# Performance work log

Measured on AMD Instinct MI355X. Metric: run time of the kernel, lower is better.

The kernel has to match this reference:

```python
import jax, jax.numpy as jnp
import numpy as np
from jax import lax

B, T = 4, 1024
V, C, H, L = 50257, 768, 12, 12
D = C // H           # head size = 64
FF = 4 * C           # ffn hidden = 3072
EPS = 1e-5


def setup_inputs() -> dict:
    key = jax.random.key(0)
    ks = jax.random.split(key, 20)
    s = 0.02
    inp = {
        'x': jax.random.randint(ks[0], (B, T), 0, V, dtype=jnp.int32),
        'y': jax.random.randint(ks[1], (B, T), 0, V, dtype=jnp.int32),
        'tok_emb': jax.random.normal(ks[2], (V, C), jnp.float32) * s,
        'pos_emb': jax.random.normal(ks[3], (V, C), jnp.float32) * s,
        'Wk': jax.random.normal(ks[4], (L, H, C, D), jnp.float32) * s,
        'Wq': jax.random.normal(ks[5], (L, H, C, D), jnp.float32) * s,
        'Wv': jax.random.normal(ks[6], (L, H, C, D), jnp.float32) * s,
        'Wproj': jax.random.normal(ks[7], (L, C, C), jnp.float32) * s,
        'bproj': jnp.zeros((L, C), jnp.float32),
        'ln1_g': jnp.ones((L, C), jnp.float32),
        'ln1_b': jnp.zeros((L, C), jnp.float32),
        'W1': jax.random.normal(ks[8], (L, C, FF), jnp.float32) * s,
        'b1': jnp.zeros((L, FF), jnp.float32),
        'W2': jax.random.normal(ks[9], (L, FF, C), jnp.float32) * s,
        'b2': jnp.zeros((L, C), jnp.float32),
        'ln2_g': jnp.ones((L, C), jnp.float32),
        'ln2_b': jnp.zeros((L, C), jnp.float32),
        'Wlm': jax.random.normal(ks[10], (C, V), jnp.float32) * s,
        'blm': jnp.zeros((V,), jnp.float32),
    }
    return inp


def _layernorm(x, g, b):
    m = jnp.mean(x, axis=-1, keepdims=True)
    v = jnp.var(x, axis=-1, keepdims=True)
    return (x - m) * lax.rsqrt(v + EPS) * g + b


def _forward(x, tok_emb, pos_emb, Wk, Wq, Wv, Wproj, bproj, ln1_g, ln1_b,
             W1, b1, W2, b2, ln2_g, ln2_b, Wlm, blm):
    # NOTE: the original indexes the position embedding table with token ids x.
    h = tok_emb[x] + pos_emb[x]                      # [B,T,C]
    mask = jnp.tril(jnp.ones((T, T), bool))          # causal tril buffer
    scale = D ** -0.5

    def layer(h, p):
        wk, wq, wv, wp, bp, g1, be1, w1, bb1, w2, bb2, g2, be2 = p
        k = jnp.einsum('btc,hcd->bhtd', h, wk)
        q = jnp.einsum('btc,hcd->bhtd', h, wq)
        v = jnp.einsum('btc,hcd->bhtd', h, wv)
        # faithful quirk: k @ q^T (rows=k index, cols=q index)
        wei = jnp.einsum('bhtd,bhsd->bhts', k, q) * scale
        wei = jnp.where(mask, wei, -jnp.inf)
        wei = jax.nn.softmax(wei, axis=-1)
        o = jnp.einsum('bhts,bhsd->bhtd', wei, v)    # [B,H,T,D]
        o = o.transpose(0, 2, 1, 3).reshape(B, T, C) # concat heads
        attn = o @ wp + bp
        h = _layernorm(h + attn, g1, be1)
        ff = jax.nn.relu(h @ w1 + bb1) @ w2 + bb2
        h = _layernorm(h + ff, g2, be2)
        return h, None

    params = (Wk, Wq, Wv, Wproj, bproj, ln1_g, ln1_b, W1, b1, W2, b2, ln2_g, ln2_b)
    h, _ = lax.scan(layer, h, params)
    logits = h @ Wlm + blm                           # [B,T,V]
    return logits


def reference(x, y, tok_emb, pos_emb, Wk, Wq, Wv, Wproj, bproj, ln1_g, ln1_b,
              W1, b1, W2, b2, ln2_g, ln2_b, Wlm, blm):
    logits = _forward(x, tok_emb, pos_emb, Wk, Wq, Wv, Wproj, bproj,
                      ln1_g, ln1_b, W1, b1, W2, b2, ln2_g, ln2_b, Wlm, blm)
    logp = jax.nn.log_softmax(logits, axis=-1)
    loss = -jnp.mean(jnp.take_along_axis(logp, y[..., None].astype(jnp.int32), axis=-1))
    return logits, loss
```

## Files before the change

### kernel.cpp

```cpp
#include <hip/hip_runtime.h>
#include <hip/hip_bf16.h>
#include <math.h>

#define BB 4
#define TT 1024
#define VV 50257
#define VPAD2 50432
#define CC 768
#define HH 12
#define DD 64
#define LL 12
#define FFH 3072
#define MROWS (BB*TT)
#define QBLK 128
#define KVBLK 64
#define NPART (VPAD2 / 64)

typedef __bf16 bf16x8 __attribute__((ext_vector_type(8)));
typedef float  f32x4  __attribute__((ext_vector_type(4)));
typedef unsigned int u32;
#define AS1 __attribute__((address_space(1)))
#define AS3 __attribute__((address_space(3)))

static __device__ __forceinline__ void gload_lds16(const void* g, void* l) {
    __builtin_amdgcn_global_load_lds((const AS1 u32*)g, (AS3 u32*)l, 16, 0, 0);
}

static __device__ __forceinline__ void stage_tile(const __hip_bfloat16* __restrict__ A,
                                                  const __hip_bfloat16* __restrict__ Bt,
                                                  int Kld, int k0, int bm, int bn,
                                                  int w, int l, char* As, char* Bs) {
    #pragma unroll
    for (int it = 0; it < 4; it++) {
        int chunk = w * 4 + it;
        int o = chunk * 1024 + l * 16;
        int row = o >> 7;
        int cb = (o & 127) ^ ((row & 7) << 4);
        gload_lds16(A + (size_t)(bm + row) * Kld + k0 + (cb >> 1), As + chunk * 1024);
        gload_lds16(Bt + (size_t)(bn + row) * Kld + k0 + (cb >> 1), Bs + chunk * 1024);
    }
}

static __device__ __forceinline__ void stage_tile256(const __hip_bfloat16* __restrict__ A,
                                                     const __hip_bfloat16* __restrict__ Bt,
                                                     int Kld, int k0, int bm, int bn,
                                                     int w, int l, char* As, char* Bs) {
    #pragma unroll
    for (int it = 0; it < 4; it++) {
        int chunk = w * 4 + it;
        int o = chunk * 1024 + l * 16;
        int row = o >> 7;
        int cb = (o & 127) ^ ((row & 7) << 4);
        gload_lds16(A + (size_t)(bm + row) * Kld + k0 + (cb >> 1), As + chunk * 1024);
        gload_lds16(Bt + (size_t)(bn + row) * Kld + k0 + (cb >> 1), Bs + chunk * 1024);
    }
}

__global__ void embed_kernel(const int* __restrict__ x, const float* __restrict__ tok,
                             const float* __restrict__ pos, float* __restrict__ h,
                             __hip_bfloat16* __restrict__ hb) {
    int idx = blockIdx.x * 256 + threadIdx.x;
    if (idx >= MROWS * CC) return;
    int row = idx / CC, c = idx - row * CC;
    int id = x[row];
    float v = tok[(size_t)id * CC + c] + pos[(size_t)id * CC + c];
    h[idx] = v;
    hb[idx] = __float2bfloat16(v);
}

__global__ __launch_bounds__(256) void cvtT_mat(const float* __restrict__ in,
                                                __hip_bfloat16* __restrict__ out,
                                                int K, int Nin,
                                                size_t ibs, size_t obs) {
    __shared__ float t[32][33];
    const float* ip = in + blockIdx.z * ibs;
    __hip_bfloat16* op = out + blockIdx.z * obs;
    int n0 = blockIdx.x * 32, k0 = blockIdx.y * 32;
    int tx = threadIdx.x & 31, ty = threadIdx.x >> 5;
    #pragma unroll
    for (int i = 0; i < 4; i++) {
        int k = k0 + ty + i * 8, n = n0 + tx;
        t[ty + i * 8][tx] = (n < Nin) ? ip[(size_t)k * Nin + n] : 0.f;
    }
    __syncthreads();
    #pragma unroll
    for (int i = 0; i < 4; i++) {
        int n = n0 + ty + i * 8, k = k0 + tx;
        op[(size_t)n * K + k] = __float2bfloat16(t[tx][ty + i * 8]);
    }
}

__global__ __launch_bounds__(256) void cvtT_qkv(const float* __restrict__ Wk,
                                                const float* __restrict__ Wq,
                                                const float* __restrict__ Wv,
                                                __hip_bfloat16* __restrict__ kT,
                                                __hip_bfloat16* __restrict__ qT,
                                                __hip_bfloat16* __restrict__ vT) {
    int z = blockIdx.z;
    int tensor = z / 144, lh = z % 144;
    int l = lh / HH, hh = lh % HH;
    const float* in = (tensor == 0 ? Wk : tensor == 1 ? Wq : Wv) + (size_t)lh * CC * DD;
    __hip_bfloat16* out = (tensor == 0 ? kT : tensor == 1 ? qT : vT)
                          + ((size_t)l * CC + hh * DD) * CC;
    __shared__ float t[32][33];
    int c0 = blockIdx.x * 32, d0 = blockIdx.y * 32;
    int tx = threadIdx.x & 31, ty = threadIdx.x >> 5;
    #pragma unroll
    for (int i = 0; i < 4; i++)
        t[ty + i * 8][tx] = in[(size_t)(c0 + ty + i * 8) * DD + d0 + tx];
    __syncthreads();
    #pragma unroll
    for (int i = 0; i < 4; i++)
        out[(size_t)(d0 + ty + i * 8) * CC + c0 + tx] = __float2bfloat16(t[tx][ty + i * 8]);
}

__global__ __launch_bounds__(256) void gemm_mfma(const __hip_bfloat16* __restrict__ A,
                                                 const __hip_bfloat16* __restrict__ Bt,
                                                 const float* __restrict__ bias,
                                                 float* __restrict__ Cf,
                                                 __hip_bfloat16* __restrict__ Cb,
                                                 int M, int N, int K, int relu) {
    __shared__ __align__(16) char smem[65536];
    int tid = threadIdx.x;
    int l = tid & 63, w = tid >> 6;
    int wr = w >> 1, wc = w & 1;
    int bm = blockIdx.y * 128, bn = blockIdx.x * 128;

    f32x4 acc[4][4] = {};

    stage_tile(A, Bt, K, 0, bm, bn, w, l, smem, smem + 32768);
    int p = 0;
    for (int k0 = 0; k0 < K; k0 += 64) {
        __syncthreads();
        if (k0 + 64 < K)
            stage_tile(A, Bt, K, k0 + 64, bm, bn, w, l,
                       smem + (p ^ 1) * 16384, smem + 32768 + (p ^ 1) * 16384);
        const char* Ab = smem + p * 16384;
        const char* Bb = smem + 32768 + p * 16384;
        #pragma unroll
        for (int ks = 0; ks < 2; ks++) {
            bf16x8 af[4], bfr[4];
            #pragma unroll
            for (int i = 0; i < 4; i++) {
                int row = wr * 64 + i * 16 + (l & 15);
                int cb = (ks * 64 + (l >> 4) * 16) ^ ((row & 7) << 4);
                af[i] = *(const bf16x8*)(Ab + row * 128 + cb);
            }
            #pragma unroll
            for (int j = 0; j < 4; j++) {
                int row = wc * 64 + j * 16 + (l & 15);
                int cb = (ks * 64 + (l >> 4) * 16) ^ ((row & 7) << 4);
                bfr[j] = *(const bf16x8*)(Bb + row * 128 + cb);
            }
            #pragma unroll
            for (int i = 0; i < 4; i++)
                #pragma unroll
                for (int j = 0; j < 4; j++)
                    acc[i][j] = __builtin_amdgcn_mfma_f32_16x16x32_bf16(af[i], bfr[j], acc[i][j], 0, 0, 0);
        }
        p ^= 1;
    }

    if (Cb) {
        __hip_bfloat16* ebh = (__hip_bfloat16*)smem;
        __syncthreads();
        #pragma unroll
        for (int i = 0; i < 4; i++) {
            #pragma unroll
            for (int j = 0; j < 4; j++) {
                int colt = wc * 64 + j * 16 + (l & 15);
                float bv = bias ? bias[bn + colt] : 0.f;
                #pragma unroll
                for (int r = 0; r < 4; r++) {
                    int rowc = wr * 64 + i * 16 + (l >> 4) * 4 + r;
                    float v = acc[i][j][r] + bv;
                    if (relu) v = fmaxf(v, 0.f);
                    ebh[rowc * 136 + colt] = __float2bfloat16(v);
                }
            }
        }
        __syncthreads();
        #pragma unroll
        for (int pass = 0; pass < 8; pass++) {
            int idx = pass * 256 + tid;
            int rowc = idx >> 4, colq = idx & 15;
            *(bf16x8*)&Cb[(size_t)(bm + rowc) * N + bn + colq * 8] =
                *(const bf16x8*)&ebh[rowc * 136 + colq * 8];
        }
    } else {
        float* eb = (float*)smem;
        #pragma unroll
        for (int c = 0; c < 2; c++) {
            __syncthreads();
            if (wr == c) {
                #pragma unroll
                for (int i = 0; i < 4; i++) {
                    #pragma unroll
                    for (int j = 0; j < 4; j++) {
                        int colt = wc * 64 + j * 16 + (l & 15);
                        float bv = bias ? bias[bn + colt] : 0.f;
                        #pragma unroll
                        for (int r = 0; r < 4; r++) {
                            int rowc = i * 16 + (l >> 4) * 4 + r;
                            float v = acc[i][j][r] + bv;
                            if (relu) v = fmaxf(v, 0.f);
                            eb[rowc * 132 + colt] = v;
                        }
                    }
                }
            }
            __syncthreads();
            #pragma unroll
            for (int pass = 0; pass < 8; pass++) {
                int idx = pass * 256 + tid;
                int rowc = idx >> 5, colq = idx & 31;
                *(f32x4*)&Cf[(size_t)(bm + c * 64 + rowc) * N + bn + colq * 4] =
                    *(const f32x4*)&eb[rowc * 132 + colq * 4];
            }
        }
    }
}

__global__ __launch_bounds__(512) void lm_head_mfma256(const __hip_bfloat16* __restrict__ A,
                                                       const __hip_bfloat16* __restrict__ Bt,
                                                       const float* __restrict__ bias,
                                                       float* __restrict__ Cf,
                                                       float* __restrict__ pm,
                                                       float* __restrict__ ps) {
    __shared__ __align__(16) char smem[131072];
    int tid = threadIdx.x;
    int l = tid & 63, w = tid >> 6;
    int wr = w >> 2, wc = w & 3;
    int bm = blockIdx.x * 256, bn = blockIdx.y * 256;

    f32x4 acc[8][4] = {};

    stage_tile256(A, Bt, CC, 0, bm, bn, w, l, smem, smem + 65536);
    int p = 0;
    for (int k0 = 0; k0 < CC; k0 += 64) {
        __syncthreads();
        if (k0 + 64 < CC)
            stage_tile256(A, Bt, CC, k0 + 64, bm, bn, w, l,
                          smem + (p ^ 1) * 32768, smem + 65536 + (p ^ 1) * 32768);
        const char* Ab = smem + p * 32768;
        const char* Bb = smem + 65536 + p * 32768;
        #pragma unroll
        for (int ks = 0; ks < 2; ks++) {
            bf16x8 af[8], bfr[4];
            #pragma unroll
            for (int i = 0; i < 8; i++) {
                int row = wr * 128 + i * 16 + (l & 15);
                int cb = (ks * 64 + (l >> 4) * 16) ^ ((row & 7) << 4);
                af[i] = *(const bf16x8*)(Ab + row * 128 + cb);
            }
            #pragma unroll
            for (int j = 0; j < 4; j++) {
                int row = wc * 64 + j * 16 + (l & 15);
                int cb = (ks * 64 + (l >> 4) * 16) ^ ((row & 7) << 4);
                bfr[j] = *(const bf16x8*)(Bb + row * 128 + cb);
            }
            #pragma unroll
            for (int i = 0; i < 8; i++)
                #pragma unroll
                for (int j = 0; j < 4; j++)
                    acc[i][j] = __builtin_amdgcn_mfma_f32_16x16x32_bf16(af[i], bfr[j], acc[i][j], 0, 0, 0);
        }
        p ^= 1;
    }

    #pragma unroll
    for (int j = 0; j < 4; j++) {
        int col = bn + wc * 64 + j * 16 + (l & 15);
        float bv = (col < VV) ? bias[col] : 0.f;
        #pragma unroll
        for (int i = 0; i < 8; i++)
            #pragma unroll
            for (int r = 0; r < 4; r++)
                acc[i][j][r] += bv;
    }

    int pidx = blockIdx.y * 4 + wc;
    #pragma unroll
    for (int i = 0; i < 8; i++) {
        int row = bm + wr * 128 + i * 16 + (l >> 4) * 4;
        #pragma unroll
        for (int r = 0; r < 4; r++) {
            float pv[4];
            float rmax = -1e30f;
            #pragma unroll
            for (int j = 0; j < 4; j++) {
                int col = bn + wc * 64 + j * 16 + (l & 15);
                float v = (col < VV) ? acc[i][j][r] : -1e30f;
                pv[j] = v;
                rmax = fmaxf(rmax, v);
            }
            #pragma unroll
            for (int msk = 1; msk < 16; msk <<= 1)
                rmax = fmaxf(rmax, __shfl_xor(rmax, msk));
            float s = 0.f;
            #pragma unroll
            for (int j = 0; j < 4; j++) s += __expf(pv[j] - rmax);
            #pragma unroll
            for (int msk = 1; msk < 16; msk <<= 1)
                s += __shfl_xor(s, msk);
            if ((l & 15) == 0) {
                pm[(size_t)(row + r) * NPART + pidx] = rmax;
                ps[(size_t)(row + r) * NPART + pidx] = s;
            }
        }
    }

    float* eb = (float*)smem;
    #pragma unroll
    for (int c = 0; c < 4; c++) {
        __syncthreads();
        if (wr == (c >> 1)) {
            int i0 = (c & 1) * 4;
            #pragma unroll
            for (int i = 0; i < 4; i++) {
                #pragma unroll
                for (int j = 0; j < 4; j++) {
                    int colt = wc * 64 + j * 16 + (l & 15);
                    #pragma unroll
                    for (int r = 0; r < 4; r++) {
                        int rowc = i * 16 + (l >> 4) * 4 + r;
                        eb[rowc * 264 + colt] = acc[i0 + i][j][r];
                    }
                }
            }
        }
        __syncthreads();
        #pragma unroll
        for (int pass = 0; pass < 32; pass++) {
            int idx = pass * 512 + tid;
            int rowc = idx >> 8, colq = idx & 255;
            int col = bn + colq;
            if (col < VV)
                Cf[(size_t)(bm + c * 64 + rowc) * VV + col] = eb[rowc * 264 + colq];
        }
    }
}

__global__ __launch_bounds__(256) void nll_combine(const float* __restrict__ pm,
                                                   const float* __restrict__ ps,
                                                   const float* __restrict__ logits,
                                                   const int* __restrict__ y,
                                                   float* __restrict__ rl) {
    int m = blockIdx.x, tid = threadIdx.x;
    __shared__ float rm[256], rs[256];
    float mt = -1e30f, st = 0.f;
    for (int i = tid; i < NPART; i += 256) {
        float mi = pm[(size_t)m * NPART + i];
        float si = ps[(size_t)m * NPART + i];
        float mn = fmaxf(mt, mi);
        st = st * __expf(mt - mn) + si * __expf(mi - mn);
        mt = mn;
    }
    rm[tid] = mt; rs[tid] = st; __syncthreads();
    for (int off = 128; off > 0; off >>= 1) {
        if (tid < off) {
            float ma = rm[tid], mb = rm[tid + off];
            float mn = fmaxf(ma, mb);
            rs[tid] = rs[tid] * __expf(ma - mn) + rs[tid + off] * __expf(mb - mn);
            rm[tid] = mn;
        }
        __syncthreads();
    }
    if (tid == 0)
        rl[m] = logf(rs[0]) + rm[0] - logits[(size_t)m * VV + y[m]];
}

__global__ __launch_bounds__(256) void gemm_qkv_mfma(const __hip_bfloat16* __restrict__ A,
                                                     const __hip_bfloat16* __restrict__ kT,
                                                     const __hip_bfloat16* __restrict__ qT,
                                                     const __hip_bfloat16* __restrict__ vT,
                                                     __hip_bfloat16* __restrict__ ko,
                                                     __hip_bfloat16* __restrict__ qo,
                                                     __hip_bfloat16* __restrict__ vto) {
    const __hip_bfloat16* Bt = (blockIdx.z == 0) ? kT : (blockIdx.z == 1) ? qT : vT;
    __shared__ __align__(16) char smem[65536];
    int tid = threadIdx.x;
    int l = tid & 63, w = tid >> 6;
    int wr = w >> 1, wc = w & 1;
    int bm = blockIdx.y * 128, bn = blockIdx.x * 128;

    f32x4 acc[4][4] = {};

    stage_tile(A, Bt, CC, 0, bm, bn, w, l, smem, smem + 32768);
    int p = 0;
    for (int k0 = 0; k0 < CC; k0 += 64) {
        __syncthreads();
        if (k0 + 64 < CC)
            stage_tile(A, Bt, CC, k0 + 64, bm, bn, w, l,
                       smem + (p ^ 1) * 16384, smem + 32768 + (p ^ 1) * 16384);
        const char* Ab = smem + p * 16384;
        const char* Bb = smem + 32768 + p * 16384;
        #pragma unroll
        for (int ks = 0; ks < 2; ks++) {
            bf16x8 af[4], bfr[4];
            #pragma unroll
            for (int i = 0; i < 4; i++) {
                int row = wr * 64 + i * 16 + (l & 15);
                int cb = (ks * 64 + (l >> 4) * 16) ^ ((row & 7) << 4);
                af[i] = *(const bf16x8*)(Ab + row * 128 + cb);
            }
            #pragma unroll
            for (int j = 0; j < 4; j++) {
                int row = wc * 64 + j * 16 + (l & 15);
                int cb = (ks * 64 + (l >> 4) * 16) ^ ((row & 7) << 4);
                bfr[j] = *(const bf16x8*)(Bb + row * 128 + cb);
            }
            #pragma unroll
            for (int i = 0; i < 4; i++)
                #pragma unroll
                for (int j = 0; j < 4; j++)
                    acc[i][j] = __builtin_amdgcn_mfma_f32_16x16x32_bf16(af[i], bfr[j], acc[i][j], 0, 0, 0);
        }
        p ^= 1;
    }
    int zz = blockIdx.z;
    #pragma unroll
    for (int i = 0; i < 4; i++) {
        int row = bm + wr * 64 + i * 16 + (l >> 4) * 4;
        #pragma unroll
        for (int j = 0; j < 4; j++) {
            int col = bn + wc * 64 + j * 16 + (l & 15);
            int head = col >> 6, d = col & 63;
            #pragma unroll
            for (int r = 0; r < 4; r++) {
                int m = row + r;
                int b = m >> 10, t = m & 1023;
                __hip_bfloat16 val = __float2bfloat16(acc[i][j][r]);
                if (zz == 0)      ko[(((size_t)(b * HH + head)) * TT + t) * DD + d] = val;
                else if (zz == 1) qo[(((size_t)(b * HH + head)) * TT + t) * DD + d] = val;
                else              vto[(((size_t)(b * HH + head)) * DD + d) * TT + t] = val;
            }
        }
    }
}

__global__ __launch_bounds__(256) void attn_mfma(const __hip_bfloat16* __restrict__ kq,
                                                 const __hip_bfloat16* __restrict__ qk,
                                                 const __hip_bfloat16* __restrict__ vt,
                                                 __hip_bfloat16* __restrict__ oc) {
    __shared__ __hip_bfloat16 Qs[2][KVBLK * 64];
    __shared__ __hip_bfloat16 Vs[2][64 * KVBLK];
    __shared__ __hip_bfloat16 Ps[QBLK * KVBLK];
    int tid = threadIdx.x;
    int l = tid & 63, w = tid >> 6;
    int t0 = blockIdx.x * QBLK;
    size_t bh = (size_t)(blockIdx.z * HH + blockIdx.y);
    const __hip_bfloat16* kqp = kq + bh * TT * DD;
    const __hip_bfloat16* qkp = qk + bh * TT * DD;
    const __hip_bfloat16* vtp = vt + bh * DD * TT;

    bf16x8 af[2][2];
    #pragma unroll
    for (int i = 0; i < 2; i++)
        #pragma unroll
        for (int ks = 0; ks < 2; ks++)
            af[i][ks] = *(const bf16x8*)&kqp[(size_t)(t0 + w * 32 + i * 16 + (l & 15)) * DD
                                             + ks * 32 + (l >> 4) * 8];

    f32x4 acc_o[2][4] = {};
    float mrow[2][4], lrow[2][4];
    #pragma unroll
    for (int i = 0; i < 2; i++)
        #pragma unroll
        for (int r = 0; r < 4; r++) { mrow[i][r] = -1e30f; lrow[i][r] = 0.f; }

    auto stageKV = [&](int pp, int s0) {
        #pragma unroll
        for (int it = 0; it < 2; it++) {
            int chunk = w * 2 + it;
            int o = chunk * 1024 + l * 16;
            int row = o >> 7;
            int cb = (o & 127) ^ ((row & 7) << 4);
            gload_lds16(qkp + (size_t)(s0 + row) * DD + (cb >> 1),
                        (char*)Qs[pp] + chunk * 1024);
            gload_lds16(vtp + (size_t)row * TT + s0 + (cb >> 1),
                        (char*)Vs[pp] + chunk * 1024);
        }
    };

    int nt = (t0 + QBLK) / KVBLK;
    stageKV(0, 0);
    int p = 0;
    for (int ti = 0; ti < nt; ti++) {
        int s0 = ti * KVBLK;
        __syncthreads();
        if (ti + 1 < nt) stageKV(p ^ 1, s0 + KVBLK);

        f32x4 sa[2][4] = {};
        #pragma unroll
        for (int ks = 0; ks < 2; ks++) {
            bf16x8 bfr[4];
            #pragma unroll
            for (int j = 0; j < 4; j++) {
                int row = j * 16 + (l & 15);
                int cb = (ks * 64 + (l >> 4) * 16) ^ ((row & 7) << 4);
                bfr[j] = *(const bf16x8*)((const char*)Qs[p] + row * 128 + cb);
            }
            #pragma unroll
            for (int i = 0; i < 2; i++)
                #pragma unroll
                for (int j = 0; j < 4; j++)
                    sa[i][j] = __builtin_amdgcn_mfma_f32_16x16x32_bf16(af[i][ks], bfr[j], sa[i][j], 0, 0, 0);
        }

        #pragma unroll
        for (int i = 0; i < 2; i++) {
            #pragma unroll
            for (int r = 0; r < 4; r++) {
                int t = t0 + w * 32 + i * 16 + (l >> 4) * 4 + r;
                float pv[4];
                float rmax = -1e30f;
                #pragma unroll
                for (int j = 0; j < 4; j++) {
                    int s = s0 + j * 16 + (l & 15);
                    float v = sa[i][j][r] * 0.125f;
                    v = (s <= t) ? v : -1e30f;
                    pv[j] = v;
                    rmax = fmaxf(rmax, v);
                }
                #pragma unroll
                for (int msk = 1; msk < 16; msk <<= 1)
                    rmax = fmaxf(rmax, __shfl_xor(rmax, msk));
                float mo = mrow[i][r];
                float mn = fmaxf(mo, rmax);
                float fac = __expf(mo - mn);
                float ls = 0.f;
                int prow = w * 32 + i * 16 + (l >> 4) * 4 + r;
                #pragma unroll
                for (int j = 0; j < 4; j++) {
                    float e = __expf(pv[j] - mn);
                    ls += e;
                    int cb = (j * 32 + (l & 15) * 2) ^ ((prow & 7) << 4);
                    *(__hip_bfloat16*)((char*)Ps + prow * 128 + cb) = __float2bfloat16(e);
                }
                #pragma unroll
                for (int msk = 1; msk < 16; msk <<= 1)
                    ls += __shfl_xor(ls, msk);
                mrow[i][r] = mn;
                lrow[i][r] = lrow[i][r] * fac + ls;
                #pragma unroll
                for (int jd = 0; jd < 4; jd++)
                    acc_o[i][jd][r] *= fac;
            }
        }

        #pragma unroll
        for (int ks = 0; ks < 2; ks++) {
            bf16x8 pa[2], vf[4];
            #pragma unroll
            for (int i = 0; i < 2; i++) {
                int row = w * 32 + i * 16 + (l & 15);
                int cb = (ks * 64 + (l >> 4) * 16) ^ ((row & 7) << 4);
                pa[i] = *(const bf16x8*)((const char*)Ps + row * 128 + cb);
            }
            #pragma unroll
            for (int jd = 0; jd < 4; jd++) {
                int row = jd * 16 + (l & 15);
                int cb = (ks * 64 + (l >> 4) * 16) ^ ((row & 7) << 4);
                vf[jd] = *(const bf16x8*)((const char*)Vs[p] + row * 128 + cb);
            }
            #pragma unroll
            for (int i = 0; i < 2; i++)
                #pragma unroll
                for (int jd = 0; jd < 4; jd++)
                    acc_o[i][jd] = __builtin_amdgcn_mfma_f32_16x16x32_bf16(pa[i], vf[jd], acc_o[i][jd], 0, 0, 0);
        }
        p ^= 1;
    }

    int b = blockIdx.z, hh = blockIdx.y;
    #pragma unroll
    for (int i = 0; i < 2; i++) {
        #pragma unroll
        for (int r = 0; r < 4; r++) {
            float inv = 1.f / lrow[i][r];
            int t = t0 + w * 32 + i * 16 + (l >> 4) * 4 + r;
            #pragma unroll
            for (int jd = 0; jd < 4; jd++) {
                int d = jd * 16 + (l & 15);
                oc[((size_t)(b * TT + t)) * CC + hh * DD + d] =
                    __float2bfloat16(acc_o[i][jd][r] * inv);
            }
        }
    }
}

__global__ __launch_bounds__(256) void resid_ln(float* __restrict__ h,
                                                const float* __restrict__ t,
                                                const float* __restrict__ g,
                                                const float* __restrict__ bta,
                                                __hip_bfloat16* __restrict__ hb) {
    int row = blockIdx.x;
    int tid = threadIdx.x;
    __shared__ float red[256];
    float x[3];
    float s = 0.f;
    #pragma unroll
    for (int i = 0; i < 3; i++) {
        int c = tid + i * 256;
        x[i] = h[(size_t)row * CC + c] + t[(size_t)row * CC + c];
        s += x[i];
    }
    red[tid] = s; __syncthreads();
    for (int off = 128; off > 0; off >>= 1) {
        if (tid < off) red[tid] += red[tid + off];
        __syncthreads();
    }
    float mean = red[0] * (1.f / CC); __syncthreads();
    float s2 = 0.f;
    #pragma unroll
    for (int i = 0; i < 3; i++) { float dd = x[i] - mean; s2 += dd * dd; }
    red[tid] = s2; __syncthreads();
    for (int off = 128; off > 0; off >>= 1) {
        if (tid < off) red[tid] += red[tid + off];
        __syncthreads();
    }
    float inv = rsqrtf(red[0] * (1.f / CC) + 1e-5f);
    #pragma unroll
    for (int i = 0; i < 3; i++) {
        int c = tid + i * 256;
        float o = (x[i] - mean) * inv * g[c] + bta[c];
        h[(size_t)row * CC + c] = o;
        hb[(size_t)row * CC + c] = __float2bfloat16(o);
    }
}

__global__ __launch_bounds__(256) void loss_reduce(const float* __restrict__ rl,
                                                   float* __restrict__ out) {
    int tid = threadIdx.x;
    __shared__ float red[256];
    float s = 0.f;
    for (int i = tid; i < MROWS; i += 256) s += rl[i];
    red[tid] = s; __syncthreads();
    for (int off = 128; off > 0; off >>= 1) {
        if (tid < off) red[tid] += red[tid + off];
        __syncthreads();
    }
    if (tid == 0) out[0] = red[0] * (1.f / MROWS);
}

extern "C" void kernel_launch(void* const* d_in, const int* in_sizes, int n_in,
                              void* d_out, int out_size, void* d_ws, size_t ws_size,
                              hipStream_t stream) {
    const int*   x     = (const int*)d_in[0];
    const int*   y     = (const int*)d_in[1];
    const float* tok   = (const float*)d_in[2];
    const float* pos   = (const float*)d_in[3];
    const float* Wk    = (const float*)d_in[4];
    const float* Wq    = (const float*)d_in[5];
    const float* Wv    = (const float*)d_in[6];
    const float* Wproj = (const float*)d_in[7];
    const float* bproj = (const float*)d_in[8];
    const float* ln1g  = (const float*)d_in[9];
    const float* ln1b  = (const float*)d_in[10];
    const float* W1    = (const float*)d_in[11];
    const float* b1    = (const float*)d_in[12];
    const float* W2    = (const float*)d_in[13];
    const float* b2    = (const float*)d_in[14];
    const float* ln2g  = (const float*)d_in[15];
    const float* ln2b  = (const float*)d_in[16];
    const float* Wlm   = (const float*)d_in[17];
    const float* blm   = (const float*)d_in[18];

    float* logits = (float*)d_out;
    float* lossp  = (float*)d_out + ((size_t)out_size - 1);

    char* p = (char*)d_ws;
    auto alloc = [&](size_t bytes) { char* r = p; p += (bytes + 255) & ~255ULL; return r; };
    const size_t S_HC = (size_t)MROWS * CC;

    float* h    = (float*)alloc(S_HC * 4);
    float* tmpf = (float*)alloc(S_HC * 4);
    float* rl   = (float*)alloc(MROWS * 4);
    float* pm   = (float*)alloc((size_t)MROWS * NPART * 4);
    float* ps   = (float*)alloc((size_t)MROWS * NPART * 4);
    __hip_bfloat16* kbb  = (__hip_bfloat16*)alloc(S_HC * 2);
    __hip_bfloat16* qbb  = (__hip_bfloat16*)alloc(S_HC * 2);
    __hip_bfloat16* vtb  = (__hip_bfloat16*)alloc(S_HC * 2);
    __hip_bfloat16* hb   = (__hip_bfloat16*)alloc(S_HC * 2);
    __hip_bfloat16* ocb  = (__hip_bfloat16*)alloc(S_HC * 2);
    __hip_bfloat16* ff1b = (__hip_bfloat16*)alloc((size_t)MROWS * FFH * 2);
    __hip_bfloat16* kT   = (__hip_bfloat16*)alloc((size_t)LL * CC * CC * 2);
    __hip_bfloat16* qT   = (__hip_bfloat16*)alloc((size_t)LL * CC * CC * 2);
    __hip_bfloat16* vT   = (__hip_bfloat16*)alloc((size_t)LL * CC * CC * 2);
    __hip_bfloat16* pT   = (__hip_bfloat16*)alloc((size_t)LL * CC * CC * 2);
    __hip_bfloat16* w1T  = (__hip_bfloat16*)alloc((size_t)LL * CC * FFH * 2);
    __hip_bfloat16* w2T  = (__hip_bfloat16*)alloc((size_t)LL * FFH * CC * 2);
    __hip_bfloat16* lmT  = (__hip_bfloat16*)alloc((size_t)VPAD2 * CC * 2);

    dim3 blk(256);

    cvtT_qkv<<<dim3(24, 2, 3 * 144), blk, 0, stream>>>(Wk, Wq, Wv, kT, qT, vT);
    cvtT_mat<<<dim3(24, 24, LL), blk, 0, stream>>>(Wproj, pT, CC, CC,
                                                   (size_t)CC * CC, (size_t)CC * CC);
    cvtT_mat<<<dim3(96, 24, LL), blk, 0, stream>>>(W1, w1T, CC, FFH,
                                                   (size_t)CC * FFH, (size_t)FFH * CC);
    cvtT_mat<<<dim3(24, 96, LL), blk, 0, stream>>>(W2, w2T, FFH, CC,
                                                   (size_t)FFH * CC, (size_t)CC * FFH);
    cvtT_mat<<<dim3(VPAD2 / 32, 24, 1), blk, 0, stream>>>(Wlm, lmT, CC, VV, 0, 0);

    embed_kernel<<<dim3((MROWS * CC + 255) / 256), blk, 0, stream>>>(x, tok, pos, h, hb);

    for (int l = 0; l < LL; l++) {
        const __hip_bfloat16* kT_l = kT + (size_t)l * CC * CC;
        const __hip_bfloat16* qT_l = qT + (size_t)l * CC * CC;
        const __hip_bfloat16* vT_l = vT + (size_t)l * CC * CC;
        const __hip_bfloat16* pT_l = pT + (size_t)l * CC * CC;
        const __hip_bfloat16* w1T_l = w1T + (size_t)l * CC * FFH;
        const __hip_bfloat16* w2T_l = w2T + (size_t)l * FFH * CC;

        gemm_qkv_mfma<<<dim3(CC / 128, MROWS / 128, 3), blk, 0, stream>>>(
            hb, kT_l, qT_l, vT_l, kbb, qbb, vtb);
        attn_mfma<<<dim3(TT / QBLK, HH, BB), blk, 0, stream>>>(kbb, qbb, vtb, ocb);
        gemm_mfma<<<dim3(CC / 128, MROWS / 128), blk, 0, stream>>>(
            ocb, pT_l, bproj + (size_t)l * CC, tmpf, (__hip_bfloat16*)nullptr,
            MROWS, CC, CC, 0);
        resid_ln<<<dim3(MROWS), blk, 0, stream>>>(h, tmpf, ln1g + (size_t)l * CC,
                                                  ln1b + (size_t)l * CC, hb);
        gemm_mfma<<<dim3(FFH / 128, MROWS / 128), blk, 0, stream>>>(
            hb, w1T_l, b1 + (size_t)l * FFH, (float*)nullptr, ff1b,
            MROWS, FFH, CC, 1);
        gemm_mfma<<<dim3(CC / 128, MROWS / 128), blk, 0, stream>>>(
            ff1b, w2T_l, b2 + (size_t)l * CC, tmpf, (__hip_bfloat16*)nullptr,
            MROWS, CC, FFH, 0);
        resid_ln<<<dim3(MROWS), blk, 0, stream>>>(h, tmpf, ln2g + (size_t)l * CC,
                                                  ln2b + (size_t)l * CC, hb);
    }

    lm_head_mfma256<<<dim3(MROWS / 256, VPAD2 / 256), dim3(512), 0, stream>>>(
        hb, lmT, blm, logits, pm, ps);
    nll_combine<<<dim3(MROWS), blk, 0, stream>>>(pm, ps, logits, y, rl);
    loss_reduce<<<dim3(1), blk, 0, stream>>>(rl, lossp);
}
```

Before: 3.394 ms.

## Halve LM-head LDS with K=32 stages and stage QKV epilogue through LDS

The LM-head GEMM now stages 32-wide K slices instead of 64, cutting its shared memory from 128KB to 64KB. The smaller footprint may let two 512-thread blocks share a CU, at the cost of twice as many barriers per K loop and a narrower swizzle. Its output epilogue is rechunked to 32-row pieces so it fits in the smaller buffer. Separately, the QKV projection epilogue now writes bf16 results into LDS and then issues 16-byte vector stores, including a transposed layout for V, replacing scattered 2-byte global stores.

```diff
diff --git a/kernel.cpp b/kernel.cpp
--- a/kernel.cpp
+++ b/kernel.cpp
@@ -41,16 +41,16 @@
     }
 }
 
-static __device__ __forceinline__ void stage_tile256(const __hip_bfloat16* __restrict__ A,
-                                                     const __hip_bfloat16* __restrict__ Bt,
-                                                     int Kld, int k0, int bm, int bn,
-                                                     int w, int l, char* As, char* Bs) {
-    #pragma unroll
-    for (int it = 0; it < 4; it++) {
-        int chunk = w * 4 + it;
+static __device__ __forceinline__ void stage_tile256_k32(const __hip_bfloat16* __restrict__ A,
+                                                         const __hip_bfloat16* __restrict__ Bt,
+                                                         int Kld, int k0, int bm, int bn,
+                                                         int w, int l, char* As, char* Bs) {
+    #pragma unroll
+    for (int it = 0; it < 2; it++) {
+        int chunk = w * 2 + it;
         int o = chunk * 1024 + l * 16;
-        int row = o >> 7;
-        int cb = (o & 127) ^ ((row & 7) << 4);
+        int row = o >> 6;
+        int cb = (o & 63) ^ ((row & 3) << 4);
         gload_lds16(A + (size_t)(bm + row) * Kld + k0 + (cb >> 1), As + chunk * 1024);
         gload_lds16(Bt + (size_t)(bn + row) * Kld + k0 + (cb >> 1), Bs + chunk * 1024);
     }
@@ -227,7 +227,7 @@
                                                        float* __restrict__ Cf,
                                                        float* __restrict__ pm,
                                                        float* __restrict__ ps) {
-    __shared__ __align__(16) char smem[131072];
+    __shared__ __align__(16) char smem[65536];
     int tid = threadIdx.x;
     int l = tid & 63, w = tid >> 6;
     int wr = w >> 2, wc = w & 3;
@@ -235,36 +235,33 @@
 
     f32x4 acc[8][4] = {};
 
-    stage_tile256(A, Bt, CC, 0, bm, bn, w, l, smem, smem + 65536);
+    stage_tile256_k32(A, Bt, CC, 0, bm, bn, w, l, smem, smem + 32768);
     int p = 0;
-    for (int k0 = 0; k0 < CC; k0 += 64) {
-        __syncthreads();
-        if (k0 + 64 < CC)
-            stage_tile256(A, Bt, CC, k0 + 64, bm, bn, w, l,
-                          smem + (p ^ 1) * 32768, smem + 65536 + (p ^ 1) * 32768);
-        const char* Ab = smem + p * 32768;
-        const char* Bb = smem + 65536 + p * 32768;
-        #pragma unroll
-        for (int ks = 0; ks < 2; ks++) {
-            bf16x8 af[8], bfr[4];
-            #pragma unroll
-            for (int i = 0; i < 8; i++) {
-                int row = wr * 128 + i * 16 + (l & 15);
-                int cb = (ks * 64 + (l >> 4) * 16) ^ ((row & 7) << 4);
-                af[i] = *(const bf16x8*)(Ab + row * 128 + cb);
-            }
-            #pragma unroll
-            for (int j = 0; j < 4; j++) {
-                int row = wc * 64 + j * 16 + (l & 15);
-                int cb = (ks * 64 + (l >> 4) * 16) ^ ((row & 7) << 4);
-                bfr[j] = *(const bf16x8*)(Bb + row * 128 + cb);
-            }
-            #pragma unroll
-            for (int i = 0; i < 8; i++)
-                #pragma unroll
-                for (int j = 0; j < 4; j++)
-                    acc[i][j] = __builtin_amdgcn_mfma_f32_16x16x32_bf16(af[i], bfr[j], acc[i][j], 0, 0, 0);
-        }
+    for (int k0 = 0; k0 < CC; k0 += 32) {
+        __syncthreads();
+        if (k0 + 32 < CC)
+            stage_tile256_k32(A, Bt, CC, k0 + 32, bm, bn, w, l,
+                              smem + (p ^ 1) * 16384, smem + 32768 + (p ^ 1) * 16384);
+        const char* Ab = smem + p * 16384;
+        const char* Bb = smem + 32768 + p * 16384;
+        bf16x8 af[8], bfr[4];
+        #pragma unroll
+        for (int i = 0; i < 8; i++) {
+            int row = wr * 128 + i * 16 + (l & 15);
+            int cb = ((l >> 4) * 16) ^ ((row & 3) << 4);
+            af[i] = *(const bf16x8*)(Ab + row * 64 + cb);
+        }
+        #pragma unroll
+        for (int j = 0; j < 4; j++) {
+            int row = wc * 64 + j * 16 + (l & 15);
+            int cb = ((l >> 4) * 16) ^ ((row & 3) << 4);
+            bfr[j] = *(const bf16x8*)(Bb + row * 64 + cb);
+        }
+        #pragma unroll
+        for (int i = 0; i < 8; i++)
+            #pragma unroll
+            for (int j = 0; j < 4; j++)
+                acc[i][j] = __builtin_amdgcn_mfma_f32_16x16x32_bf16(af[i], bfr[j], acc[i][j], 0, 0, 0);
         p ^= 1;
     }
 
@@ -312,31 +309,31 @@
 
     float* eb = (float*)smem;
     #pragma unroll
-    for (int c = 0; c < 4; c++) {
-        __syncthreads();
-        if (wr == (c >> 1)) {
-            int i0 = (c & 1) * 4;
-            #pragma unroll
-            for (int i = 0; i < 4; i++) {
+    for (int c = 0; c < 8; c++) {
+        __syncthreads();
+        if (wr == (c >> 2)) {
+            int i0 = (c & 3) * 2;
+            #pragma unroll
+            for (int ii = 0; ii < 2; ii++) {
                 #pragma unroll
                 for (int j = 0; j < 4; j++) {
                     int colt = wc * 64 + j * 16 + (l & 15);
                     #pragma unroll
                     for (int r = 0; r < 4; r++) {
-                        int rowc = i * 16 + (l >> 4) * 4 + r;
-                        eb[rowc * 264 + colt] = acc[i0 + i][j][r];
+                        int rowc = ii * 16 + (l >> 4) * 4 + r;
+                        eb[rowc * 264 + colt] = acc[i0 + ii][j][r];
                     }
                 }
             }
         }
         __syncthreads();
         #pragma unroll
-        for (int pass = 0; pass < 32; pass++) {
+        for (int pass = 0; pass < 16; pass++) {
             int idx = pass * 512 + tid;
             int rowc = idx >> 8, colq = idx & 255;
             int col = bn + colq;
             if (col < VV)
-                Cf[(size_t)(bm + c * 64 + rowc) * VV + col] = eb[rowc * 264 + colq];
+                Cf[(size_t)(bm + c * 32 + rowc) * VV + col] = eb[rowc * 264 + colq];
         }
     }
 }
@@ -418,23 +415,56 @@
         }
         p ^= 1;
     }
+
     int zz = blockIdx.z;
-    #pragma unroll
-    for (int i = 0; i < 4; i++) {
-        int row = bm + wr * 64 + i * 16 + (l >> 4) * 4;
-        #pragma unroll
-        for (int j = 0; j < 4; j++) {
-            int col = bn + wc * 64 + j * 16 + (l & 15);
-            int head = col >> 6, d = col & 63;
-            #pragma unroll
-            for (int r = 0; r < 4; r++) {
-                int m = row + r;
-                int b = m >> 10, t = m & 1023;
-                __hip_bfloat16 val = __float2bfloat16(acc[i][j][r]);
-                if (zz == 0)      ko[(((size_t)(b * HH + head)) * TT + t) * DD + d] = val;
-                else if (zz == 1) qo[(((size_t)(b * HH + head)) * TT + t) * DD + d] = val;
-                else              vto[(((size_t)(b * HH + head)) * DD + d) * TT + t] = val;
-            }
+    int b = bm >> 10, tbase = bm & 1023;
+    __hip_bfloat16* eb = (__hip_bfloat16*)smem;
+    __syncthreads();
+    if (zz != 2) {
+        #pragma unroll
+        for (int i = 0; i < 4; i++)
+            #pragma unroll
+            for (int j = 0; j < 4; j++) {
+                int colt = wc * 64 + j * 16 + (l & 15);
+                #pragma unroll
+                for (int r = 0; r < 4; r++) {
+                    int rowc = wr * 64 + i * 16 + (l >> 4) * 4 + r;
+                    eb[rowc * 136 + colt] = __float2bfloat16(acc[i][j][r]);
+                }
+            }
+        __syncthreads();
+        __hip_bfloat16* O = (zz == 0) ? ko : qo;
+        #pragma unroll
+        for (int pass = 0; pass < 8; pass++) {
+            int idx = pass * 256 + tid;
+            int rowc = idx >> 4, colq = idx & 15;
+            int head = (bn >> 6) + (colq >> 3);
+            int d = (colq & 7) * 8;
+            int t = tbase + rowc;
+            *(bf16x8*)&O[(((size_t)(b * HH + head)) * TT + t) * DD + d] =
+                *(const bf16x8*)&eb[rowc * 136 + colq * 8];
+        }
+    } else {
+        #pragma unroll
+        for (int i = 0; i < 4; i++)
+            #pragma unroll
+            for (int j = 0; j < 4; j++) {
+                int colt = wc * 64 + j * 16 + (l & 15);
+                #pragma unroll
+                for (int r = 0; r < 4; r++) {
+                    int rowc = wr * 64 + i * 16 + (l >> 4) * 4 + r;
+                    eb[colt * 136 + rowc] = __float2bfloat16(acc[i][j][r]);
+                }
+            }
+        __syncthreads();
+        #pragma unroll
+        for (int pass = 0; pass < 8; pass++) {
+            int idx = pass * 256 + tid;
+            int line = idx >> 4, tq = idx & 15;
+            int head = (bn >> 6) + (line >> 6);
+            int d = line & 63;
+            *(bf16x8*)&vto[(((size_t)(b * HH + head)) * DD + d) * TT + tbase + tq * 8] =
+                *(const bf16x8*)&eb[line * 136 + tq * 8];
         }
     }
 }
```

New measurement: 3.336 ms. No clear change (-1.7%).
